# Kernel tuning notes

Hardware: AMD Instinct MI355X
Metric: run time of the kernel (lower is better)

## Reference

```python
import jax, jax.numpy as jnp
import numpy as np

B, I, H = 4096, 512, 1024


def setup_inputs() -> dict:
    key = jax.random.key(0)
    ks = jax.random.split(key, 22)
    inp = {
        "y": jax.random.normal(ks[0], (B, I), jnp.float32),
        "h_light": jax.random.normal(ks[1], (B, H), jnp.float32),
        "c_light": jax.random.normal(ks[2], (B, H), jnp.float32),
        "h_temp": jax.random.normal(ks[3], (B, H), jnp.float32),
        "c_temp": jax.random.normal(ks[4], (B, H), jnp.float32),
    }
    names = ["w_f_light", "w_i_light", "w_c_light", "w_o_light",
             "w_f_light_temp", "w_i_light_temp", "w_c_light_temp", "w_o_light_temp"]
    for j, n in enumerate(names):
        inp[n] = jax.random.normal(ks[5 + j], (H, H + I), jnp.float32) * 0.02
        inp["b" + n[1:]] = jax.random.normal(ks[13 + j], (H,), jnp.float32) * 0.02
    return inp


def _branch(hx, wf, bf, wi, bi, wc, bc, wo, bo):
    # Fuse the 4 gate GEMMs of one branch into a single [B, H+I] x [H+I, 4H] matmul
    W = jnp.concatenate([wf, wi, wc, wo], axis=0)            # [4H, H+I]
    b = jnp.concatenate([bf, bi, bc, bo], axis=0)            # [4H]
    z = hx @ W.T + b                                         # [B, 4H]
    zf, zi, zc, zo = jnp.split(z, 4, axis=1)
    return jax.nn.sigmoid(zf), jax.nn.sigmoid(zi), jnp.tanh(zc), jax.nn.sigmoid(zo)


def reference(y, h_light, c_light, h_temp, c_temp,
              w_f_light, b_f_light, w_i_light, b_i_light,
              w_c_light, b_c_light, w_o_light, b_o_light,
              w_f_light_temp, b_f_light_temp, w_i_light_temp, b_i_light_temp,
              w_c_light_temp, b_c_light_temp, w_o_light_temp, b_o_light_temp):
    hx_l = jnp.concatenate([h_light, y], axis=1)  # [B, H+I]
    hx_t = jnp.concatenate([h_temp, y], axis=1)   # [B, H+I]
    f1, i1, ch1, o1 = _branch(hx_l, w_f_light, b_f_light, w_i_light, b_i_light,
                              w_c_light, b_c_light, w_o_light, b_o_light)
    f2, i2, ch2, o2 = _branch(hx_t, w_f_light_temp, b_f_light_temp, w_i_light_temp,
                              b_i_light_temp, w_c_light_temp, b_c_light_temp,
                              w_o_light_temp, b_o_light_temp)
    c_new = (f1 * c_light + i1 * ch1) + (f2 * c_light + i2 * ch2)
    h_new = (o1 + o2) * jnp.tanh(c_new)
    return h_new, c_new
```

## Files before the change

### kernel.cpp

```cpp
#include <hip/hip_runtime.h>
#include <stdint.h>


#define B_DIM 4096
#define I_DIM 512
#define H_DIM 1024
#define K_DIM 1536
#define NK 48
#define BUFB (48 * 1024)

typedef __attribute__((ext_vector_type(8))) __bf16 bf16x8;
typedef __attribute__((ext_vector_type(4))) float f32x4;
typedef __attribute__((ext_vector_type(4))) uint32_t u32x4;

static __device__ __forceinline__ uint32_t f2bf(float f) {
  uint32_t u = __builtin_bit_cast(uint32_t, f);
  return (u + 0x7FFFu + ((u >> 16) & 1u)) >> 16;
}
static __device__ __forceinline__ uint32_t pack2(float lo, float hi) {
  return f2bf(lo) | (f2bf(hi) << 16);
}
static __device__ __forceinline__ float sigf(float x) {
  return 1.f / (1.f + __expf(-x));
}
static __device__ __forceinline__ float tanhfast(float x) {
  float t = __expf(fminf(2.f * x, 80.f));
  return (t - 1.f) / (t + 1.f);
}

__global__ __launch_bounds__(192) void convert_kernel(
    const float* __restrict__ y, const float* __restrict__ h_light,
    const float* __restrict__ h_temp,
    const float* __restrict__ w0, const float* __restrict__ w1,
    const float* __restrict__ w2, const float* __restrict__ w3,
    const float* __restrict__ w4, const float* __restrict__ w5,
    const float* __restrict__ w6, const float* __restrict__ w7,
    uint16_t* __restrict__ ws)
{
  const int row_all = blockIdx.x;
  const int cs = threadIdx.x;
  const int cl = (cs & ~3) | ((cs & 3) ^ ((row_all >> 1) & 3));
  const int k0 = cl * 8;
  const float* src;
  if (row_all < 2 * B_DIM) {
    const int branch = row_all >> 12;
    const int row = row_all & (B_DIM - 1);
    const float* hb = branch ? h_temp : h_light;
    src = (k0 < H_DIM) ? (hb + (size_t)row * H_DIM + k0)
                       : (y + (size_t)row * I_DIM + (k0 - H_DIM));
  } else {
    const int ra = row_all - 2 * B_DIM;
    const int mat = ra >> 10;
    const int row = ra & (H_DIM - 1);
    const float* w = (mat < 4) ? ((mat < 2) ? (mat == 0 ? w0 : w1) : (mat == 2 ? w2 : w3))
                               : ((mat < 6) ? (mat == 4 ? w4 : w5) : (mat == 6 ? w6 : w7));
    src = w + (size_t)row * K_DIM + k0;
  }
  f32x4 v0 = *(const f32x4*)src;
  f32x4 v1 = *(const f32x4*)(src + 4);
  u32x4 o;
  o[0] = pack2(v0[0], v0[1]);
  o[1] = pack2(v0[2], v0[3]);
  o[2] = pack2(v1[0], v1[1]);
  o[3] = pack2(v1[2], v1[3]);
  *(u32x4*)(ws + ((size_t)row_all * 192 + cs) * 8) = o;
}

__global__ __launch_bounds__(512, 2) void lstm_fused_kernel(
    const uint16_t* __restrict__ ws,
    const float* __restrict__ c_light,
    const float* __restrict__ bf1, const float* __restrict__ bi1,
    const float* __restrict__ bc1, const float* __restrict__ bo1,
    const float* __restrict__ bf2, const float* __restrict__ bi2,
    const float* __restrict__ bc2, const float* __restrict__ bo2,
    float* __restrict__ out)
{
  __shared__ alignas(128) char smem[3 * BUFB];

  const int tid = threadIdx.x;
  const int lane = tid & 63;
  const int wv = tid >> 6;

  const int bid = blockIdx.x;
  const int xcd = bid & 7;
  const int slot = bid >> 3;
  const int bm0 = (slot & 31) * 128;
  const int bn0 = (xcd * 2 + (slot >> 5)) * 64;

  const uint16_t* wsA = ws;
  const uint16_t* wsW = ws + (size_t)2 * B_DIM * K_DIM;

  const int rA = lane & 15;
  const int kg = lane >> 4;
  const uint32_t fo = (uint32_t)rA * 64u + (uint32_t)((kg ^ ((rA >> 1) & 3))) * 16u;

  const uint16_t* sA0;
  const uint16_t* sA1;
  const uint16_t* sB[4];
  {
    int c = tid;
    sA0 = wsA + (size_t)(bm0 + ((c >> 2) & 127)) * K_DIM + (c & 3) * 8;
    c = 512 + tid;
    sA1 = wsA + (size_t)B_DIM * K_DIM + (size_t)(bm0 + ((c >> 2) & 127)) * K_DIM + (c & 3) * 8;
#pragma unroll
    for (int j = 0; j < 4; ++j) {
      int c2 = j * 512 + tid;
      sB[j] = wsW + (size_t)(c2 >> 8) * ((size_t)H_DIM * K_DIM) +
              (size_t)(bn0 + ((c2 >> 2) & 63)) * K_DIM + (c2 & 3) * 8;
    }
  }
  const uint32_t ldA0 = (uint32_t)tid * 16u;
  const uint32_t ldA1 = (uint32_t)(512 + tid) * 16u;
  uint32_t ldB[4];
#pragma unroll
  for (int j = 0; j < 4; ++j) ldB[j] = (uint32_t)(1024 + j * 512 + tid) * 16u;

  const uint32_t aBase = (uint32_t)(wv >> 2) * 8192u;
  const uint32_t bBase = 16384u + (uint32_t)wv * 4096u;

#define ISSUE(srcp, ldsoff, tg)                                              \
  __builtin_amdgcn_global_load_lds(                                          \
      (const __attribute__((address_space(1))) void*)(srcp),                 \
      (__attribute__((address_space(3))) void*)(&smem[(size_t)(tg)*BUFB + (ldsoff)]), \
      16, 0, 0)

  f32x4 acc[8][4];
#pragma unroll
  for (int m = 0; m < 8; ++m)
#pragma unroll
    for (int n = 0; n < 4; ++n) acc[m][n] = (f32x4){0.f, 0.f, 0.f, 0.f};

  ISSUE(sA0, ldA0, 0); ISSUE(sA1, ldA1, 0);
#pragma unroll
  for (int j = 0; j < 4; ++j) ISSUE(sB[j], ldB[j], 0);
  ISSUE(sA0 + 32, ldA0, 1); ISSUE(sA1 + 32, ldA1, 1);
#pragma unroll
  for (int j = 0; j < 4; ++j) ISSUE(sB[j] + 32, ldB[j], 1);
  sA0 += 64; sA1 += 64;
#pragma unroll
  for (int j = 0; j < 4; ++j) sB[j] += 64;

  for (int kt = 0; kt < NK; ++kt) {
    if (kt < NK - 1) asm volatile("s_waitcnt vmcnt(6)" ::: "memory");
    else             asm volatile("s_waitcnt vmcnt(0)" ::: "memory");
    __builtin_amdgcn_s_barrier();

    const int bi = kt % 3;
    const char* As = smem + (size_t)bi * BUFB + aBase;
    const char* Bs = smem + (size_t)bi * BUFB + bBase;

    bf16x8 Af[8], Bf[4];
#pragma unroll
    for (int m = 0; m < 8; ++m) Af[m] = *(const bf16x8*)(As + m * 1024 + fo);
#pragma unroll
    for (int n = 0; n < 4; ++n) Bf[n] = *(const bf16x8*)(Bs + n * 1024 + fo);

    if (kt + 2 < NK) {
      const int tg = (bi == 0) ? 2 : bi - 1;
      ISSUE(sA0, ldA0, tg);   ISSUE(sA1, ldA1, tg);
      ISSUE(sB[0], ldB[0], tg); ISSUE(sB[1], ldB[1], tg);
      ISSUE(sB[2], ldB[2], tg); ISSUE(sB[3], ldB[3], tg);
      sA0 += 32; sA1 += 32;
#pragma unroll
      for (int j = 0; j < 4; ++j) sB[j] += 32;
    }

    __builtin_amdgcn_s_setprio(1);
#pragma unroll
    for (int m = 0; m < 8; ++m)
#pragma unroll
      for (int n = 0; n < 4; ++n)
        acc[m][n] = __builtin_amdgcn_mfma_f32_16x16x32_bf16(Af[m], Bf[n], acc[m][n], 0, 0, 0);
    __builtin_amdgcn_s_setprio(0);
  }
#undef ISSUE

  float* zst = (float*)smem;
#pragma unroll
  for (int q = 0; q < 4; ++q) {
    __syncthreads();
#pragma unroll
    for (int mm = 0; mm < 2; ++mm)
#pragma unroll
      for (int n = 0; n < 4; ++n)
#pragma unroll
        for (int j = 0; j < 4; ++j) {
          int r = mm * 16 + kg * 4 + j;
          int c = n * 16 + rA;
          zst[wv * 2176 + r * 68 + c] = acc[q * 2 + mm][n][j];
        }
    __syncthreads();

    int r = tid >> 4;
    int cb = (tid & 15) * 4;
    int grow = bm0 + q * 32 + r;
    int gc = bn0 + cb;
    const float* zb = zst + r * 68 + cb;
    f32x4 z0 = *(const f32x4*)(zb + 0 * 2176) + *(const f32x4*)(bf1 + gc);
    f32x4 z1 = *(const f32x4*)(zb + 1 * 2176) + *(const f32x4*)(bi1 + gc);
    f32x4 z2 = *(const f32x4*)(zb + 2 * 2176) + *(const f32x4*)(bc1 + gc);
    f32x4 z3 = *(const f32x4*)(zb + 3 * 2176) + *(const f32x4*)(bo1 + gc);
    f32x4 z4 = *(const f32x4*)(zb + 4 * 2176) + *(const f32x4*)(bf2 + gc);
    f32x4 z5 = *(const f32x4*)(zb + 5 * 2176) + *(const f32x4*)(bi2 + gc);
    f32x4 z6 = *(const f32x4*)(zb + 6 * 2176) + *(const f32x4*)(bc2 + gc);
    f32x4 z7 = *(const f32x4*)(zb + 7 * 2176) + *(const f32x4*)(bo2 + gc);
    f32x4 cl4 = *(const f32x4*)(c_light + (size_t)grow * H_DIM + gc);
    f32x4 hv, cv;
#pragma unroll
    for (int j = 0; j < 4; ++j) {
      float f1 = sigf(z0[j]);
      float i1 = sigf(z1[j]);
      float ch1 = tanhfast(z2[j]);
      float o1 = sigf(z3[j]);
      float f2 = sigf(z4[j]);
      float i2 = sigf(z5[j]);
      float ch2 = tanhfast(z6[j]);
      float o2 = sigf(z7[j]);
      float cn = f1 * cl4[j] + i1 * ch1 + f2 * cl4[j] + i2 * ch2;
      hv[j] = (o1 + o2) * tanhfast(cn);
      cv[j] = cn;
    }
    *(f32x4*)(out + (size_t)grow * H_DIM + gc) = hv;
    *(f32x4*)(out + (size_t)(B_DIM * H_DIM) + (size_t)grow * H_DIM + gc) = cv;
  }
}

extern "C" void kernel_launch(void* const* d_in, const int* in_sizes, int n_in,
                              void* d_out, int out_size, void* d_ws, size_t ws_size,
                              hipStream_t stream) {
  (void)in_sizes; (void)n_in; (void)out_size; (void)ws_size;
  const float* y       = (const float*)d_in[0];
  const float* h_light = (const float*)d_in[1];
  const float* c_light = (const float*)d_in[2];
  const float* h_temp  = (const float*)d_in[3];
  uint16_t* ws = (uint16_t*)d_ws;

  convert_kernel<<<16384, 192, 0, stream>>>(
      y, h_light, h_temp,
      (const float*)d_in[5],  (const float*)d_in[7],  (const float*)d_in[9],  (const float*)d_in[11],
      (const float*)d_in[13], (const float*)d_in[15], (const float*)d_in[17], (const float*)d_in[19],
      ws);

  lstm_fused_kernel<<<512, 512, 0, stream>>>(
      ws, c_light,
      (const float*)d_in[6],  (const float*)d_in[8],  (const float*)d_in[10], (const float*)d_in[12],
      (const float*)d_in[14], (const float*)d_in[16], (const float*)d_in[18], (const float*)d_in[20],
      (float*)d_out);
}
```

Measured before the change: 307.8 us.

## Load per-wave B weight fragments straight to registers, bypassing LDS staging

Each wave already used only its own gate's B slice, so the B operand is now read directly from global memory into registers. The next k-step's fragment is prefetched while the current one feeds the MFMAs, and the async global-to-LDS path now carries only the A tile. This removes B's LDS write/read traffic, cuts the LDS footprint, and drops the swizzle from the weight conversion. The cost is exposed global latency on the B fragments, with only a one-step register prefetch to hide it, plus extra VGPR pressure from the double-buffered B registers.

```diff
diff --git a/kernel.cpp b/kernel.cpp
--- a/kernel.cpp
+++ b/kernel.cpp
@@ -7,7 +7,7 @@
 #define H_DIM 1024
 #define K_DIM 1536
 #define NK 48
-#define BUFB (48 * 1024)
+#define ABUFB (16 * 1024)
 
 typedef __attribute__((ext_vector_type(8))) __bf16 bf16x8;
 typedef __attribute__((ext_vector_type(4))) float f32x4;
@@ -39,22 +39,24 @@
 {
   const int row_all = blockIdx.x;
   const int cs = threadIdx.x;
-  const int cl = (cs & ~3) | ((cs & 3) ^ ((row_all >> 1) & 3));
-  const int k0 = cl * 8;
   const float* src;
+  int cl;
   if (row_all < 2 * B_DIM) {
+    cl = (cs & ~3) | ((cs & 3) ^ ((row_all >> 1) & 3));
+    const int k0 = cl * 8;
     const int branch = row_all >> 12;
     const int row = row_all & (B_DIM - 1);
     const float* hb = branch ? h_temp : h_light;
     src = (k0 < H_DIM) ? (hb + (size_t)row * H_DIM + k0)
                        : (y + (size_t)row * I_DIM + (k0 - H_DIM));
   } else {
+    cl = cs;
     const int ra = row_all - 2 * B_DIM;
     const int mat = ra >> 10;
     const int row = ra & (H_DIM - 1);
     const float* w = (mat < 4) ? ((mat < 2) ? (mat == 0 ? w0 : w1) : (mat == 2 ? w2 : w3))
                                : ((mat < 6) ? (mat == 4 ? w4 : w5) : (mat == 6 ? w6 : w7));
-    src = w + (size_t)row * K_DIM + k0;
+    src = w + (size_t)row * K_DIM + cl * 8;
   }
   f32x4 v0 = *(const f32x4*)src;
   f32x4 v1 = *(const f32x4*)(src + 4);
@@ -75,7 +77,7 @@
     const float* __restrict__ bc2, const float* __restrict__ bo2,
     float* __restrict__ out)
 {
-  __shared__ alignas(128) char smem[3 * BUFB];
+  __shared__ alignas(128) char smem[69632];
 
   const int tid = threadIdx.x;
   const int lane = tid & 63;
@@ -92,36 +94,29 @@
 
   const int rA = lane & 15;
   const int kg = lane >> 4;
-  const uint32_t fo = (uint32_t)rA * 64u + (uint32_t)((kg ^ ((rA >> 1) & 3))) * 16u;
-
-  const uint16_t* sA0;
-  const uint16_t* sA1;
-  const uint16_t* sB[4];
-  {
-    int c = tid;
-    sA0 = wsA + (size_t)(bm0 + ((c >> 2) & 127)) * K_DIM + (c & 3) * 8;
-    c = 512 + tid;
-    sA1 = wsA + (size_t)B_DIM * K_DIM + (size_t)(bm0 + ((c >> 2) & 127)) * K_DIM + (c & 3) * 8;
-#pragma unroll
-    for (int j = 0; j < 4; ++j) {
-      int c2 = j * 512 + tid;
-      sB[j] = wsW + (size_t)(c2 >> 8) * ((size_t)H_DIM * K_DIM) +
-              (size_t)(bn0 + ((c2 >> 2) & 63)) * K_DIM + (c2 & 3) * 8;
-    }
-  }
-  const uint32_t ldA0 = (uint32_t)tid * 16u;
-  const uint32_t ldA1 = (uint32_t)(512 + tid) * 16u;
-  uint32_t ldB[4];
-#pragma unroll
-  for (int j = 0; j < 4; ++j) ldB[j] = (uint32_t)(1024 + j * 512 + tid) * 16u;
-
-  const uint32_t aBase = (uint32_t)(wv >> 2) * 8192u;
-  const uint32_t bBase = 16384u + (uint32_t)wv * 4096u;
-
-#define ISSUE(srcp, ldsoff, tg)                                              \
+  const uint32_t fo = (uint32_t)rA * 64u + (uint32_t)(kg ^ ((rA >> 1) & 3)) * 16u;
+  const uint32_t aoff = (uint32_t)(wv >> 2) * 8192u + fo;
+
+  const uint16_t* sA[2];
+  uint32_t ldA[2];
+#pragma unroll
+  for (int i = 0; i < 2; ++i) {
+    int c = i * 512 + tid;
+    sA[i] = wsA + (size_t)(c >> 9) * ((size_t)B_DIM * K_DIM) +
+            (size_t)(bm0 + ((c >> 2) & 127)) * K_DIM + (c & 3) * 8;
+    ldA[i] = (uint32_t)c * 16u;
+  }
+
+  const uint16_t* pB[4];
+#pragma unroll
+  for (int n = 0; n < 4; ++n)
+    pB[n] = wsW + (size_t)wv * ((size_t)H_DIM * K_DIM) +
+            (size_t)(bn0 + n * 16 + rA) * K_DIM + kg * 8;
+
+#define ISSUE(srcp, ldsoff, buf)                                             \
   __builtin_amdgcn_global_load_lds(                                          \
       (const __attribute__((address_space(1))) void*)(srcp),                 \
-      (__attribute__((address_space(3))) void*)(&smem[(size_t)(tg)*BUFB + (ldsoff)]), \
+      (__attribute__((address_space(3))) void*)(smem + (buf)*ABUFB + (ldsoff)), \
       16, 0, 0)
 
   f32x4 acc[8][4];
@@ -130,39 +125,36 @@
 #pragma unroll
     for (int n = 0; n < 4; ++n) acc[m][n] = (f32x4){0.f, 0.f, 0.f, 0.f};
 
-  ISSUE(sA0, ldA0, 0); ISSUE(sA1, ldA1, 0);
-#pragma unroll
-  for (int j = 0; j < 4; ++j) ISSUE(sB[j], ldB[j], 0);
-  ISSUE(sA0 + 32, ldA0, 1); ISSUE(sA1 + 32, ldA1, 1);
-#pragma unroll
-  for (int j = 0; j < 4; ++j) ISSUE(sB[j] + 32, ldB[j], 1);
-  sA0 += 64; sA1 += 64;
-#pragma unroll
-  for (int j = 0; j < 4; ++j) sB[j] += 64;
+  ISSUE(sA[0], ldA[0], 0); ISSUE(sA[1], ldA[1], 0);
+  ISSUE(sA[0] + 32, ldA[0], 1); ISSUE(sA[1] + 32, ldA[1], 1);
+  sA[0] += 64; sA[1] += 64;
+  asm volatile("" ::: "memory");
+  bf16x8 Bcur[4], Bnxt[4];
+#pragma unroll
+  for (int n = 0; n < 4; ++n) { Bcur[n] = *(const bf16x8*)pB[n]; pB[n] += 32; }
 
   for (int kt = 0; kt < NK; ++kt) {
     if (kt < NK - 1) asm volatile("s_waitcnt vmcnt(6)" ::: "memory");
     else             asm volatile("s_waitcnt vmcnt(0)" ::: "memory");
     __builtin_amdgcn_s_barrier();
 
-    const int bi = kt % 3;
-    const char* As = smem + (size_t)bi * BUFB + aBase;
-    const char* Bs = smem + (size_t)bi * BUFB + bBase;
-
-    bf16x8 Af[8], Bf[4];
-#pragma unroll
-    for (int m = 0; m < 8; ++m) Af[m] = *(const bf16x8*)(As + m * 1024 + fo);
-#pragma unroll
-    for (int n = 0; n < 4; ++n) Bf[n] = *(const bf16x8*)(Bs + n * 1024 + fo);
-
+    const char* As = smem + (kt % 3) * ABUFB + aoff;
+    bf16x8 Af[8];
+#pragma unroll
+    for (int m = 0; m < 8; ++m) Af[m] = *(const bf16x8*)(As + m * 1024);
+
+    if (kt + 1 < NK) {
+#pragma unroll
+      for (int n = 0; n < 4; ++n) { Bnxt[n] = *(const bf16x8*)pB[n]; pB[n] += 32; }
+    } else {
+#pragma unroll
+      for (int n = 0; n < 4; ++n) Bnxt[n] = Bcur[n];
+    }
+    asm volatile("" ::: "memory");
     if (kt + 2 < NK) {
-      const int tg = (bi == 0) ? 2 : bi - 1;
-      ISSUE(sA0, ldA0, tg);   ISSUE(sA1, ldA1, tg);
-      ISSUE(sB[0], ldB[0], tg); ISSUE(sB[1], ldB[1], tg);
-      ISSUE(sB[2], ldB[2], tg); ISSUE(sB[3], ldB[3], tg);
-      sA0 += 32; sA1 += 32;
-#pragma unroll
-      for (int j = 0; j < 4; ++j) sB[j] += 32;
+      const int tg3 = (kt + 2) % 3;
+      ISSUE(sA[0], ldA[0], tg3); ISSUE(sA[1], ldA[1], tg3);
+      sA[0] += 32; sA[1] += 32;
     }
 
     __builtin_amdgcn_s_setprio(1);
@@ -170,8 +162,10 @@
     for (int m = 0; m < 8; ++m)
 #pragma unroll
       for (int n = 0; n < 4; ++n)
-        acc[m][n] = __builtin_amdgcn_mfma_f32_16x16x32_bf16(Af[m], Bf[n], acc[m][n], 0, 0, 0);
+        acc[m][n] = __builtin_amdgcn_mfma_f32_16x16x32_bf16(Af[m], Bcur[n], acc[m][n], 0, 0, 0);
     __builtin_amdgcn_s_setprio(0);
+#pragma unroll
+    for (int n = 0; n < 4; ++n) Bcur[n] = Bnxt[n];
   }
 #undef ISSUE
 
```

After: 348.2 us. 1.13x slower.
